# Kernel optimization log

Hardware: AMD Instinct MI355X
Metric: run time of the kernel (lower is better)

Reference implementation:

```python
import jax, jax.numpy as jnp
import numpy as np

B, S, H, UNITS = 32, 2048, 1024, 128

def setup_inputs() -> dict:
    key = jax.random.key(0)
    k1, k2, k3 = jax.random.split(key, 3)
    hidden_states = jax.random.normal(k1, (B, S, H), dtype=jnp.float32)
    # Dense(hidden_size, use_bias=False): weight [H, H]
    w_score = jax.random.normal(k2, (H, H), dtype=jnp.float32) * (1.0 / np.sqrt(H))
    # Dense(units, use_bias=False): weight [2H, units]
    w_out = jax.random.normal(k3, (2 * H, UNITS), dtype=jnp.float32) * (1.0 / np.sqrt(2 * H))
    return {"hidden_states": hidden_states, "w_score": w_score, "w_out": w_out}

def reference(hidden_states, w_score, w_out):
    # dense_score: [B,S,H] @ [H,H] -> [B,S,H]
    dense_score = jnp.einsum('bsh,hk->bsk', hidden_states, w_score)
    h_t = hidden_states[:, -1, :]                       # [B,H] last hidden state
    score = jnp.einsum('bh,bsh->bs', h_t, dense_score)  # attention scores [B,S]
    attn = jax.nn.softmax(score, axis=-1)               # [B,S]
    context = jnp.einsum('bsh,bs->bh', hidden_states, attn)  # [B,H]
    pre = jnp.concatenate([context, h_t], axis=-1)      # [B,2H]
    return jnp.tanh(pre @ w_out)                        # [B,units]
```

## Files before the change

### kernel.cpp

```cpp
#include <hip/hip_runtime.h>
#include <math.h>

#define B_ 32
#define S_ 2048
#define H_ 1024
#define U_ 128

#define OFF_VPART 0u
#define OFF_V     262144u
#define OFF_PM    294912u
#define OFF_PL    296960u
#define OFF_PCTX  299008u
#define OFF_CTX   2396160u
#define OFF_DPART 2428928u

__global__ __launch_bounds__(256) void k_vpart(const float* __restrict__ hid,
                                               const float* __restrict__ W,
                                               float* __restrict__ ws) {
    __shared__ float ht[32][128];
    const int t  = threadIdx.x;
    const int h0 = blockIdx.x * 64;
    const int k0 = blockIdx.y * 128;
    #pragma unroll
    for (int i = 0; i < 4; ++i) {
        int f4 = i * 256 + t;
        int bl = f4 >> 5;
        int k4 = f4 & 31;
        float4 src = *(const float4*)(hid + ((size_t)bl * S_ + (S_ - 1)) * H_ + k0 + k4 * 4);
        *(float4*)&ht[bl][k4 * 4] = src;
    }
    __syncthreads();
    const int hl = t & 63;
    const int g  = t >> 6;
    const int h  = h0 + hl;
    float acc[8];
    #pragma unroll
    for (int i = 0; i < 8; ++i) acc[i] = 0.f;
    const float4* Wr = (const float4*)(W + (size_t)h * H_ + k0);
    for (int k4 = 0; k4 < 32; ++k4) {
        float4 w4 = Wr[k4];
        float wv[4] = {w4.x, w4.y, w4.z, w4.w};
        #pragma unroll
        for (int c = 0; c < 4; ++c) {
            float w = wv[c];
            int kk = k4 * 4 + c;
            #pragma unroll
            for (int bb = 0; bb < 8; ++bb)
                acc[bb] += w * ht[g * 8 + bb][kk];
        }
    }
    float* vpart = ws + OFF_VPART;
    const int kc = blockIdx.y;
    #pragma unroll
    for (int bb = 0; bb < 8; ++bb)
        vpart[((size_t)kc * 32 + (g * 8 + bb)) * H_ + h] = acc[bb];
}

__global__ __launch_bounds__(256) void k_vreduce(float* __restrict__ ws) {
    int e = blockIdx.x * 256 + threadIdx.x;
    const float* vp = ws + OFF_VPART;
    float s = 0.f;
    #pragma unroll
    for (int kc = 0; kc < 8; ++kc) s += vp[kc * 32768 + e];
    ws[OFF_V + e] = s;
}

__global__ __launch_bounds__(256) void k_flash(const float* __restrict__ hid,
                                               float* __restrict__ ws) {
    const int t    = threadIdx.x;
    const int lane = t & 63;
    const int wave = t >> 6;
    const int b    = blockIdx.x >> 4;
    const int wi   = (blockIdx.x & 15) * 4 + wave;
    const int s0   = wi * 32;

    const float* vrow = ws + OFF_V + (size_t)b * H_;
    float4 v4[4], c4[4];
    #pragma unroll
    for (int j = 0; j < 4; ++j) {
        v4[j] = *(const float4*)(vrow + j * 256 + lane * 4);
        c4[j] = make_float4(0.f, 0.f, 0.f, 0.f);
    }
    float m = -INFINITY, l = 0.f;
    const float* base = hid + (size_t)b * S_ * H_;

    for (int r = 0; r < 32; ++r) {
        const float* row = base + (size_t)(s0 + r) * H_;
        float4 h4[4];
        #pragma unroll
        for (int j = 0; j < 4; ++j)
            h4[j] = *(const float4*)(row + j * 256 + lane * 4);
        float p = 0.f;
        #pragma unroll
        for (int j = 0; j < 4; ++j)
            p += h4[j].x * v4[j].x + h4[j].y * v4[j].y + h4[j].z * v4[j].z + h4[j].w * v4[j].w;
        #pragma unroll
        for (int off = 32; off > 0; off >>= 1) p += __shfl_xor(p, off, 64);
        if (p > m) {
            float alpha = __expf(m - p);
            l *= alpha;
            #pragma unroll
            for (int j = 0; j < 4; ++j) {
                c4[j].x *= alpha; c4[j].y *= alpha; c4[j].z *= alpha; c4[j].w *= alpha;
            }
            m = p;
        }
        float e = __expf(p - m);
        l += e;
        #pragma unroll
        for (int j = 0; j < 4; ++j) {
            c4[j].x += e * h4[j].x; c4[j].y += e * h4[j].y;
            c4[j].z += e * h4[j].z; c4[j].w += e * h4[j].w;
        }
    }
    const int pid = b * 64 + wi;
    float* pctx = ws + OFF_PCTX + (size_t)pid * H_;
    #pragma unroll
    for (int j = 0; j < 4; ++j)
        *(float4*)(pctx + j * 256 + lane * 4) = c4[j];
    if (lane == 0) { ws[OFF_PM + pid] = m; ws[OFF_PL + pid] = l; }
}

__global__ __launch_bounds__(256) void k_merge(float* __restrict__ ws) {
    const int b = blockIdx.x;
    const int t = threadIdx.x;
    const float* pm = ws + OFF_PM + b * 64;
    const float* pl = ws + OFF_PL + b * 64;
    float M = -INFINITY;
    for (int i = 0; i < 64; ++i) M = fmaxf(M, pm[i]);
    float L = 0.f;
    float4 c = make_float4(0.f, 0.f, 0.f, 0.f);
    const float* pctx = ws + OFF_PCTX + (size_t)b * 64 * H_;
    for (int i = 0; i < 64; ++i) {
        float w = __expf(pm[i] - M);
        L += pl[i] * w;
        float4 x = *(const float4*)(pctx + (size_t)i * H_ + t * 4);
        c.x += w * x.x; c.y += w * x.y; c.z += w * x.z; c.w += w * x.w;
    }
    float inv = 1.f / L;
    c.x *= inv; c.y *= inv; c.z *= inv; c.w *= inv;
    *(float4*)(ws + OFF_CTX + (size_t)b * H_ + t * 4) = c;
}

__global__ __launch_bounds__(128) void k_out_part(const float* __restrict__ hid,
                                                  const float* __restrict__ W2,
                                                  float* __restrict__ ws) {
    __shared__ float pre[256];
    const int jc = blockIdx.x;
    const int b  = blockIdx.y;
    const int t  = threadIdx.x;
    #pragma unroll
    for (int i = 0; i < 2; ++i) {
        int idx = t * 2 + i;
        int j = jc * 256 + idx;
        float val = (j < 1024)
            ? ws[OFF_CTX + (size_t)b * H_ + j]
            : hid[((size_t)b * S_ + (S_ - 1)) * H_ + (j - 1024)];
        pre[idx] = val;
    }
    __syncthreads();
    float acc = 0.f;
    const float* w2 = W2 + (size_t)jc * 256 * U_ + t;
    #pragma unroll 8
    for (int jj = 0; jj < 256; ++jj)
        acc += pre[jj] * w2[(size_t)jj * U_];
    ws[OFF_DPART + ((size_t)jc * 32 + b) * U_ + t] = acc;
}

__global__ __launch_bounds__(256) void k_out_final(const float* __restrict__ ws,
                                                   float* __restrict__ out) {
    int idx = blockIdx.x * 256 + threadIdx.x;
    float s = 0.f;
    #pragma unroll
    for (int jc = 0; jc < 8; ++jc) s += ws[OFF_DPART + jc * 4096 + idx];
    out[idx] = tanhf(s);
}

extern "C" void kernel_launch(void* const* d_in, const int* in_sizes, int n_in,
                              void* d_out, int out_size, void* d_ws, size_t ws_size,
                              hipStream_t stream) {
    const float* hid = (const float*)d_in[0];
    const float* W   = (const float*)d_in[1];
    const float* W2  = (const float*)d_in[2];
    float* ws  = (float*)d_ws;
    float* out = (float*)d_out;

    hipLaunchKernelGGL(k_vpart,     dim3(16, 8), dim3(256), 0, stream, hid, W, ws);
    hipLaunchKernelGGL(k_vreduce,   dim3(128),   dim3(256), 0, stream, ws);
    hipLaunchKernelGGL(k_flash,     dim3(512),   dim3(256), 0, stream, hid, ws);
    hipLaunchKernelGGL(k_merge,     dim3(32),    dim3(256), 0, stream, ws);
    hipLaunchKernelGGL(k_out_part,  dim3(8, 32), dim3(128), 0, stream, hid, W2, ws);
    hipLaunchKernelGGL(k_out_final, dim3(16),    dim3(256), 0, stream, ws, out);
}
```

Baseline: 401.1 us.

## Split flash pass into more waves, unroll two rows, use nontemporal loads

```diff
diff --git a/kernel.cpp b/kernel.cpp
--- a/kernel.cpp
+++ b/kernel.cpp
@@ -9,10 +9,17 @@
 #define OFF_VPART 0u
 #define OFF_V     262144u
 #define OFF_PM    294912u
-#define OFF_PL    296960u
-#define OFF_PCTX  299008u
-#define OFF_CTX   2396160u
-#define OFF_DPART 2428928u
+#define OFF_PL    299008u
+#define OFF_PCTX  303104u
+#define OFF_CTX   4497408u
+#define OFF_DPART 4530176u
+
+typedef float vfloat4 __attribute__((ext_vector_type(4)));
+
+static __device__ __forceinline__ float4 ntload4(const float* p) {
+    vfloat4 v = __builtin_nontemporal_load((const vfloat4*)p);
+    return make_float4(v.x, v.y, v.z, v.w);
+}
 
 __global__ __launch_bounds__(256) void k_vpart(const float* __restrict__ hid,
                                                const float* __restrict__ W,
@@ -70,9 +77,9 @@
     const int t    = threadIdx.x;
     const int lane = t & 63;
     const int wave = t >> 6;
-    const int b    = blockIdx.x >> 4;
-    const int wi   = (blockIdx.x & 15) * 4 + wave;
-    const int s0   = wi * 32;
+    const int b    = blockIdx.x >> 5;
+    const int wi   = (blockIdx.x & 31) * 4 + wave;
+    const int s0   = wi * 16;
 
     const float* vrow = ws + OFF_V + (size_t)b * H_;
     float4 v4[4], c4[4];
@@ -82,38 +89,48 @@
         c4[j] = make_float4(0.f, 0.f, 0.f, 0.f);
     }
     float m = -INFINITY, l = 0.f;
-    const float* base = hid + (size_t)b * S_ * H_;
-
-    for (int r = 0; r < 32; ++r) {
-        const float* row = base + (size_t)(s0 + r) * H_;
-        float4 h4[4];
-        #pragma unroll
-        for (int j = 0; j < 4; ++j)
-            h4[j] = *(const float4*)(row + j * 256 + lane * 4);
-        float p = 0.f;
-        #pragma unroll
-        for (int j = 0; j < 4; ++j)
-            p += h4[j].x * v4[j].x + h4[j].y * v4[j].y + h4[j].z * v4[j].z + h4[j].w * v4[j].w;
-        #pragma unroll
-        for (int off = 32; off > 0; off >>= 1) p += __shfl_xor(p, off, 64);
-        if (p > m) {
-            float alpha = __expf(m - p);
+    const float* base = hid + ((size_t)b * S_ + s0) * H_ + lane * 4;
+
+    for (int r = 0; r < 16; r += 2) {
+        const float* r0 = base + (size_t)r * H_;
+        const float* r1 = r0 + H_;
+        float4 a4[4], b4[4];
+        #pragma unroll
+        for (int j = 0; j < 4; ++j) a4[j] = ntload4(r0 + j * 256);
+        #pragma unroll
+        for (int j = 0; j < 4; ++j) b4[j] = ntload4(r1 + j * 256);
+        float p0 = 0.f, p1 = 0.f;
+        #pragma unroll
+        for (int j = 0; j < 4; ++j) {
+            p0 += a4[j].x * v4[j].x + a4[j].y * v4[j].y + a4[j].z * v4[j].z + a4[j].w * v4[j].w;
+            p1 += b4[j].x * v4[j].x + b4[j].y * v4[j].y + b4[j].z * v4[j].z + b4[j].w * v4[j].w;
+        }
+        #pragma unroll
+        for (int off = 32; off > 0; off >>= 1) {
+            p0 += __shfl_xor(p0, off, 64);
+            p1 += __shfl_xor(p1, off, 64);
+        }
+        float pmax = fmaxf(p0, p1);
+        if (pmax > m) {
+            float alpha = __expf(m - pmax);
             l *= alpha;
             #pragma unroll
             for (int j = 0; j < 4; ++j) {
                 c4[j].x *= alpha; c4[j].y *= alpha; c4[j].z *= alpha; c4[j].w *= alpha;
             }
-            m = p;
-        }
-        float e = __expf(p - m);
-        l += e;
+            m = pmax;
+        }
+        float e0 = __expf(p0 - m), e1 = __expf(p1 - m);
+        l += e0 + e1;
         #pragma unroll
         for (int j = 0; j < 4; ++j) {
-            c4[j].x += e * h4[j].x; c4[j].y += e * h4[j].y;
-            c4[j].z += e * h4[j].z; c4[j].w += e * h4[j].w;
-        }
-    }
-    const int pid = b * 64 + wi;
+            c4[j].x += e0 * a4[j].x + e1 * b4[j].x;
+            c4[j].y += e0 * a4[j].y + e1 * b4[j].y;
+            c4[j].z += e0 * a4[j].z + e1 * b4[j].z;
+            c4[j].w += e0 * a4[j].w + e1 * b4[j].w;
+        }
+    }
+    const int pid = b * 128 + wi;
     float* pctx = ws + OFF_PCTX + (size_t)pid * H_;
     #pragma unroll
     for (int j = 0; j < 4; ++j)
@@ -122,24 +139,23 @@
 }
 
 __global__ __launch_bounds__(256) void k_merge(float* __restrict__ ws) {
-    const int b = blockIdx.x;
-    const int t = threadIdx.x;
-    const float* pm = ws + OFF_PM + b * 64;
-    const float* pl = ws + OFF_PL + b * 64;
+    const int cc = blockIdx.x;
+    const int b  = blockIdx.y;
+    const int t  = threadIdx.x;
+    const float* pm = ws + OFF_PM + b * 128;
+    const float* pl = ws + OFF_PL + b * 128;
     float M = -INFINITY;
-    for (int i = 0; i < 64; ++i) M = fmaxf(M, pm[i]);
-    float L = 0.f;
-    float4 c = make_float4(0.f, 0.f, 0.f, 0.f);
-    const float* pctx = ws + OFF_PCTX + (size_t)b * 64 * H_;
-    for (int i = 0; i < 64; ++i) {
+    #pragma unroll 8
+    for (int i = 0; i < 128; ++i) M = fmaxf(M, pm[i]);
+    float L = 0.f, c = 0.f;
+    const float* pctx = ws + OFF_PCTX + (size_t)b * 128 * H_ + cc * 256 + t;
+    #pragma unroll 4
+    for (int i = 0; i < 128; ++i) {
         float w = __expf(pm[i] - M);
         L += pl[i] * w;
-        float4 x = *(const float4*)(pctx + (size_t)i * H_ + t * 4);
-        c.x += w * x.x; c.y += w * x.y; c.z += w * x.z; c.w += w * x.w;
-    }
-    float inv = 1.f / L;
-    c.x *= inv; c.y *= inv; c.z *= inv; c.w *= inv;
-    *(float4*)(ws + OFF_CTX + (size_t)b * H_ + t * 4) = c;
+        c += w * pctx[(size_t)i * H_];
+    }
+    ws[OFF_CTX + (size_t)b * H_ + cc * 256 + t] = c / L;
 }
 
 __global__ __launch_bounds__(128) void k_out_part(const float* __restrict__ hid,
@@ -187,8 +203,8 @@
 
     hipLaunchKernelGGL(k_vpart,     dim3(16, 8), dim3(256), 0, stream, hid, W, ws);
     hipLaunchKernelGGL(k_vreduce,   dim3(128),   dim3(256), 0, stream, ws);
-    hipLaunchKernelGGL(k_flash,     dim3(512),   dim3(256), 0, stream, hid, ws);
-    hipLaunchKernelGGL(k_merge,     dim3(32),    dim3(256), 0, stream, ws);
+    hipLaunchKernelGGL(k_flash,     dim3(1024),  dim3(256), 0, stream, hid, ws);
+    hipLaunchKernelGGL(k_merge,     dim3(4, 32), dim3(256), 0, stream, ws);
     hipLaunchKernelGGL(k_out_part,  dim3(8, 32), dim3(128), 0, stream, hid, W2, ws);
     hipLaunchKernelGGL(k_out_final, dim3(16),    dim3(256), 0, stream, ws, out);
 }
```

After: 391.2 us. -2.5%, faster.
